# Kernel tuning notes

Hardware: AMD Instinct MI355X
Metric: run time of the kernel (lower is better)

## Reference

```python
import jax, jax.numpy as jnp
import numpy as np

B, C_IN, C_OUT, H, W = 32, 256, 256, 32, 32


def setup_inputs() -> dict:
    key = jax.random.key(0)
    kx, kw, kb = jax.random.split(key, 3)
    x = jax.random.normal(kx, (B, C_IN, H, W), dtype=jnp.float32)
    # 1x1 conv == pointwise linear over channels: weight [out_c, in_c], bias [out_c]
    conv_w = jax.random.normal(kw, (C_OUT, C_IN), dtype=jnp.float32) * (1.0 / np.sqrt(C_IN))
    conv_b = jax.random.normal(kb, (C_OUT,), dtype=jnp.float32) * 0.01
    return {"x": x, "conv_w": conv_w, "conv_b": conv_b}


def reference(x, conv_w, conv_b):
    b, c, h, w = x.shape
    hw = h * w
    q = x.reshape(b, c, hw)  # q == k == flattened x
    # score[b,i,j] = sum_c q[b,c,i] * q[b,c,j]  -> (b, hw, hw)
    score = jnp.einsum('bci,bcj->bij', q, q)
    attn = jax.nn.softmax(score, axis=-1)
    # 1x1 conv V projection: (b, out_c, h, w)
    v = jnp.einsum('oc,bchw->bohw', conv_w, x) + conv_b[None, :, None, None]
    v = v.reshape(b, -1, hw).transpose(0, 2, 1)  # (b, hw, out_c)
    out = jnp.einsum('bij,bjo->bio', attn, v)  # (b, hw, out_c)
    # torch does .transpose(-1,-1) (a no-op) then reshape(b,-1,h,w) in row-major
    out = out.reshape(b, -1, h, w)  # (b, out_c, h, w), position-major flatten as in torch
    # MaxPool2d(2): 2x2 windows, stride 2
    oc = out.shape[1]
    out = out.reshape(b, oc, h // 2, 2, w // 2, 2).max(axis=(3, 5))
    return out
```

## Files before the change

kernel.cpp:

```cpp
#include <hip/hip_runtime.h>
#include <math.h>

#define BB 32
#define CC 256
#define NN 1024
#define KSTR 264
#define PSTR 40
#define THR 8.0f

typedef unsigned short u16;
typedef u16 u16x8 __attribute__((ext_vector_type(8)));
typedef _Float16 h16;
typedef h16 h16x8 __attribute__((ext_vector_type(8)));
typedef h16 h16x4 __attribute__((ext_vector_type(4)));
typedef float f32x4 __attribute__((ext_vector_type(4)));

__device__ __forceinline__ h16x8 ldh8(const u16* p) {
    return __builtin_bit_cast(h16x8, *(const u16x8*)p);
}
__device__ __forceinline__ f32x4 mfma16(h16x8 a, h16x8 b, f32x4 c) {
    return __builtin_amdgcn_mfma_f32_16x16x32_f16(a, b, c, 0, 0, 0);
}

__global__ __launch_bounds__(256) void k_wprep(const float* __restrict__ w,
                                               u16* __restrict__ whf) {
    int s = blockIdx.x * 256 + threadIdx.x;
    int ot = s >> 9, ks = (s >> 6) & 7, l = s & 63;
    const float* src = w + (size_t)(ot * 16 + (l & 15)) * CC + ks * 32 + 8 * (l >> 4);
    float4 a = *(const float4*)src;
    float4 c = *(const float4*)(src + 4);
    u16x8 o;
    o[0] = __builtin_bit_cast(u16, (h16)a.x); o[1] = __builtin_bit_cast(u16, (h16)a.y);
    o[2] = __builtin_bit_cast(u16, (h16)a.z); o[3] = __builtin_bit_cast(u16, (h16)a.w);
    o[4] = __builtin_bit_cast(u16, (h16)c.x); o[5] = __builtin_bit_cast(u16, (h16)c.y);
    o[6] = __builtin_bit_cast(u16, (h16)c.z); o[7] = __builtin_bit_cast(u16, (h16)c.w);
    *(u16x8*)(whf + (size_t)s * 8) = o;
}

__global__ __launch_bounds__(256) void k_split(const float* __restrict__ x,
                                               u16* __restrict__ qf) {
    __shared__ float lds[64][65];
    int bid = blockIdx.x;
    int b = bid >> 6, ct = (bid >> 4) & 3, pt = bid & 15;
    int t = threadIdx.x;
    int c0 = ct * 64, p0 = pt * 64;
    const float* xb = x + ((size_t)b * CC + c0) * NN + p0;
#pragma unroll
    for (int it = 0; it < 4; ++it) {
        int cl = (t >> 4) + it * 16;
        int pl = (t & 15) * 4;
        float4 v = *(const float4*)(xb + (size_t)cl * NN + pl);
        lds[pl + 0][cl] = v.x;
        lds[pl + 1][cl] = v.y;
        lds[pl + 2][cl] = v.z;
        lds[pl + 3][cl] = v.w;
    }
    __syncthreads();
    u16* qb = qf + ((size_t)b * NN + p0) * CC + c0;
#pragma unroll
    for (int it = 0; it < 2; ++it) {
        int pl = (t >> 3) + it * 32;
        int cl = (t & 7) * 8;
        u16x8 hv;
#pragma unroll
        for (int e = 0; e < 8; ++e) hv[e] = __builtin_bit_cast(u16, (h16)lds[pl][cl + e]);
        *(u16x8*)(qb + (size_t)pl * CC + cl) = hv;
    }
}

__global__ __launch_bounds__(256, 2) void k_vgemm(const u16* __restrict__ qf,
                                                  const u16* __restrict__ whf,
                                                  const float* __restrict__ bias,
                                                  u16* __restrict__ vf) {
    __shared__ __align__(16) u16 smem[18432];
    int bid = blockIdx.x;
    int b = bid >> 4, pt = bid & 15;
    int t = threadIdx.x;
    int wave = t >> 6, lane = t & 63;
    int l15 = lane & 15, l4 = lane >> 4;
    int p0 = pt * 64, o0 = wave * 64;

#pragma unroll
    for (int it = 0; it < 8; ++it) {
        int sidx = t + it * 256;
        int row = sidx >> 5, ch = (sidx & 31) * 8;
        *(u16x8*)&smem[row * KSTR + ch] =
            *(const u16x8*)(qf + ((size_t)b * NN + p0 + row) * CC + ch);
    }
    __syncthreads();

    f32x4 acc[4][4];
#pragma unroll
    for (int m = 0; m < 4; ++m)
#pragma unroll
        for (int n = 0; n < 4; ++n) acc[m][n] = (f32x4){0.f, 0.f, 0.f, 0.f};
#pragma unroll
    for (int ks = 0; ks < 8; ++ks) {
        h16x8 afr[4], bfr[4];
#pragma unroll
        for (int m = 0; m < 4; ++m)
            afr[m] = ldh8(whf + (size_t)(((wave * 4 + m) * 8 + ks) * 64 + lane) * 8);
#pragma unroll
        for (int n = 0; n < 4; ++n)
            bfr[n] = ldh8(&smem[(n * 16 + l15) * KSTR + ks * 32 + 8 * l4]);
#pragma unroll
        for (int m = 0; m < 4; ++m)
#pragma unroll
            for (int n = 0; n < 4; ++n) acc[m][n] = mfma16(afr[m], bfr[n], acc[m][n]);
    }
    __syncthreads();

    u16* Vs = smem + wave * 4608;
#pragma unroll
    for (int m = 0; m < 4; ++m) {
#pragma unroll
        for (int r = 0; r < 4; ++r) {
            int ol = m * 16 + 4 * l4 + r;
            float bv = bias[o0 + ol];
#pragma unroll
            for (int n = 0; n < 4; ++n)
                Vs[ol * 72 + n * 16 + l15] =
                    __builtin_bit_cast(u16, (h16)(acc[m][n][r] + bv));
        }
    }
#pragma unroll
    for (int m = 0; m < 4; ++m) {
#pragma unroll
        for (int jtl = 0; jtl < 2; ++jtl) {
            u16x8 v = *(u16x8*)&Vs[(m * 16 + l15) * 72 + jtl * 32 + 8 * l4];
            size_t idx = (((size_t)b * 32 + pt * 2 + jtl) * 16 + wave * 4 + m) * 512 +
                         lane * 8;
            *(u16x8*)(vf + idx) = v;
        }
    }
}

#define SMEM_BYTES 39424
__global__ __launch_bounds__(256, 2) void k_attn(const u16* __restrict__ qf,
                                                 const u16* __restrict__ vf,
                                                 float* __restrict__ out) {
    __shared__ __align__(16) char smem[SMEM_BYTES];
    u16* Kt = (u16*)smem;
    u16* Pt = (u16*)(smem + 33792);
    float* Sc = (float*)(smem + 38912);

    int bid = blockIdx.x;
    int xcd = bid & 7, s0 = bid >> 3;
    int b = xcd * 4 + (s0 >> 4);
    int iblk = s0 & 15;
    int i0 = iblk * 64;
    int t = threadIdx.x;
    int wave = t >> 6, lane = t & 63;
    int l15 = lane & 15, l4 = lane >> 4;
    int iw = i0 + wave * 16;

    const u16* qb = qf + (size_t)b * NN * CC;
    const u16* vfb = vf + (size_t)b * (32 * 16 * 512);

    h16x8 qfr[8];
#pragma unroll
    for (int ks = 0; ks < 8; ++ks)
        qfr[ks] = ldh8(qb + (size_t)(iw + l15) * CC + ks * 32 + 8 * l4);

    f32x4 oacc[16];
#pragma unroll
    for (int i = 0; i < 16; ++i) oacc[i] = (f32x4){0.f, 0.f, 0.f, 0.f};
    float m = -INFINITY, l = 0.f;

    {
        u16x8 kp[4];
#pragma unroll
        for (int p = 0; p < 4; ++p) {
            int sidx = t + p * 256;
            kp[p] = *(const u16x8*)(qb + (size_t)(sidx >> 5) * CC + (sidx & 31) * 8);
        }
#pragma unroll
        for (int p = 0; p < 4; ++p) {
            int sidx = t + p * 256;
            *(u16x8*)&Kt[(sidx >> 5) * KSTR + (sidx & 31) * 8] = kp[p];
        }
    }
    __syncthreads();

    u16* Pw = Pt + wave * 16 * PSTR;
    float* Scw = Sc + wave * 16;

    for (int jt = 0; jt < 32; ++jt) {
        int cur = jt & 1;
        int j0 = jt * 32;
        const u16* Kc = Kt + cur * (32 * KSTR) + l15 * KSTR + 8 * l4;

        u16x8 vfr[16];
#pragma unroll
        for (int of = 0; of < 16; ++of)
            vfr[of] = *(const u16x8*)(vfb + ((size_t)(jt * 16 + of) * 512 + lane * 8));

        u16x8 kp[4];
        if (jt < 31) {
#pragma unroll
            for (int p = 0; p < 4; ++p) {
                int sidx = t + p * 256;
                kp[p] = *(const u16x8*)(qb + (size_t)(j0 + 32 + (sidx >> 5)) * CC +
                                        (sidx & 31) * 8);
            }
        }

        f32x4 s0v = (f32x4){0.f, 0.f, 0.f, 0.f};
        f32x4 s1v = (f32x4){0.f, 0.f, 0.f, 0.f};
#pragma unroll
        for (int ks = 0; ks < 8; ++ks) {
            h16x8 a0 = ldh8(Kc + ks * 32);
            h16x8 a1 = ldh8(Kc + 16 * KSTR + ks * 32);
            s0v = mfma16(a0, qfr[ks], s0v);
            s1v = mfma16(a1, qfr[ks], s1v);
        }

        float mx = fmaxf(fmaxf(fmaxf(s0v[0], s0v[1]), fmaxf(s0v[2], s0v[3])),
                         fmaxf(fmaxf(s1v[0], s1v[1]), fmaxf(s1v[2], s1v[3])));
        mx = fmaxf(mx, __shfl_xor(mx, 16));
        mx = fmaxf(mx, __shfl_xor(mx, 32));
        if (__any(mx > m + THR)) {
            float mnew = fmaxf(m, mx);
            float sc = __expf(m - mnew);
            m = mnew;
            l *= sc;
            Scw[l15] = sc;
            f32x4 s4 = *(f32x4*)&Scw[4 * l4];
#pragma unroll
            for (int of = 0; of < 16; ++of)
#pragma unroll
                for (int r = 0; r < 4; ++r) oacc[of][r] *= s4[r];
        }
        float p0 = __expf(s0v[0] - m), p1 = __expf(s0v[1] - m);
        float p2 = __expf(s0v[2] - m), p3 = __expf(s0v[3] - m);
        float p4 = __expf(s1v[0] - m), p5 = __expf(s1v[1] - m);
        float p6 = __expf(s1v[2] - m), p7 = __expf(s1v[3] - m);
        float rs = ((p0 + p1) + (p2 + p3)) + ((p4 + p5) + (p6 + p7));
        rs += __shfl_xor(rs, 16);
        rs += __shfl_xor(rs, 32);
        l += rs;

        h16x4 pk0 = {(h16)p0, (h16)p1, (h16)p2, (h16)p3};
        h16x4 pk1 = {(h16)p4, (h16)p5, (h16)p6, (h16)p7};
        *(h16x4*)(Pw + l15 * PSTR + 4 * l4) = pk0;
        *(h16x4*)(Pw + l15 * PSTR + 16 + 4 * l4) = pk1;
        h16x8 pa = ldh8(Pw + l15 * PSTR + 8 * l4);

#pragma unroll
        for (int of = 0; of < 16; ++of)
            oacc[of] = mfma16(pa, __builtin_bit_cast(h16x8, vfr[of]), oacc[of]);

        if (jt < 31) {
#pragma unroll
            for (int p = 0; p < 4; ++p) {
                int sidx = t + p * 256;
                *(u16x8*)&Kt[(cur ^ 1) * (32 * KSTR) + (sidx >> 5) * KSTR +
                             (sidx & 31) * 8] = kp[p];
            }
            __syncthreads();
        }
    }

    {
        float inv = 1.0f / l;
        Scw[l15] = inv;
        f32x4 inv4 = *(f32x4*)&Scw[4 * l4];
#pragma unroll
        for (int of = 0; of < 16; ++of)
#pragma unroll
            for (int r = 0; r < 4; ++r) oacc[of][r] *= inv4[r];
    }

    float* Old = (float*)smem;
#pragma unroll
    for (int half = 0; half < 2; ++half) {
        __syncthreads();
        if ((wave >> 1) == half) {
            int wrow = (wave & 1) * 16;
#pragma unroll
            for (int of = 0; of < 16; ++of)
#pragma unroll
                for (int r = 0; r < 4; ++r)
                    Old[(wrow + 4 * l4 + r) * 260 + of * 16 + l15] = oacc[of][r];
        }
        __syncthreads();
#pragma unroll
        for (int it = 0; it < 8; ++it) {
            int q = it * 16 + (t >> 4);
            int ill = q >> 2, pl = q & 3, pw = t & 15;
            const float* row = &Old[ill * 260];
            int ob = pl * 64 + pw * 2;
            float mx = fmaxf(fmaxf(row[ob], row[ob + 1]),
                             fmaxf(row[ob + 32], row[ob + 33]));
            int i = i0 + half * 32 + ill;
            out[(((size_t)b * CC + (i >> 2)) * 16 + (i & 3) * 4 + pl) * 16 + pw] = mx;
        }
    }
}

extern "C" void kernel_launch(void* const* d_in, const int* in_sizes, int n_in,
                              void* d_out, int out_size, void* d_ws, size_t ws_size,
                              hipStream_t stream) {
    const float* x = (const float*)d_in[0];
    const float* w = (const float*)d_in[1];
    const float* bias = (const float*)d_in[2];
    float* out = (float*)d_out;
    u16* qf = (u16*)d_ws;
    u16* vf = qf + (size_t)BB * NN * CC;
    u16* whf = vf + (size_t)BB * NN * CC;
    k_wprep<<<32, 256, 0, stream>>>(w, whf);
    k_split<<<2048, 256, 0, stream>>>(x, qf);
    k_vgemm<<<512, 256, 0, stream>>>(qf, whf, bias, vf);
    k_attn<<<512, 256, 0, stream>>>(qf, vf, out);
}
```

Baseline: 147.6 us.

## Fuse transpose/convert with V projection and stage K via direct global-to-LDS loads

Merges the x transpose/fp16 conversion kernel and the V-projection GEMM into a single kernel. It computes V directly from fp32 x tiles held in LDS, which removes one launch and the round trip through qf for the GEMM. In the attention kernel, K tiles are now staged with global_load_lds into an unpadded, XOR-swizzled layout instead of going through registers, which frees VGPRs and drops the explicit LDS stores. The risks are the swizzle's bank-conflict behaviour and the vmcnt/barrier ordering needed before the async LDS writes become visible.

```diff
diff --git a/kernel.cpp b/kernel.cpp
--- a/kernel.cpp
+++ b/kernel.cpp
@@ -4,11 +4,12 @@
 #define BB 32
 #define CC 256
 #define NN 1024
-#define KSTR 264
+#define KSTR 256
 #define PSTR 40
 #define THR 8.0f
 
 typedef unsigned short u16;
+typedef unsigned int u32;
 typedef u16 u16x8 __attribute__((ext_vector_type(8)));
 typedef _Float16 h16;
 typedef h16 h16x8 __attribute__((ext_vector_type(8)));
@@ -20,6 +21,10 @@
 }
 __device__ __forceinline__ f32x4 mfma16(h16x8 a, h16x8 b, f32x4 c) {
     return __builtin_amdgcn_mfma_f32_16x16x32_f16(a, b, c, 0, 0, 0);
+}
+__device__ __forceinline__ void gll16(const void* g, void* l) {
+    __builtin_amdgcn_global_load_lds((const __attribute__((address_space(1))) u32*)g,
+                                     (__attribute__((address_space(3))) u32*)l, 16, 0, 0);
 }
 
 __global__ __launch_bounds__(256) void k_wprep(const float* __restrict__ w,
@@ -37,126 +42,121 @@
     *(u16x8*)(whf + (size_t)s * 8) = o;
 }
 
-__global__ __launch_bounds__(256) void k_split(const float* __restrict__ x,
-                                               u16* __restrict__ qf) {
-    __shared__ float lds[64][65];
-    int bid = blockIdx.x;
-    int b = bid >> 6, ct = (bid >> 4) & 3, pt = bid & 15;
-    int t = threadIdx.x;
-    int c0 = ct * 64, p0 = pt * 64;
-    const float* xb = x + ((size_t)b * CC + c0) * NN + p0;
-#pragma unroll
-    for (int it = 0; it < 4; ++it) {
-        int cl = (t >> 4) + it * 16;
-        int pl = (t & 15) * 4;
-        float4 v = *(const float4*)(xb + (size_t)cl * NN + pl);
-        lds[pl + 0][cl] = v.x;
-        lds[pl + 1][cl] = v.y;
-        lds[pl + 2][cl] = v.z;
-        lds[pl + 3][cl] = v.w;
-    }
-    __syncthreads();
-    u16* qb = qf + ((size_t)b * NN + p0) * CC + c0;
-#pragma unroll
-    for (int it = 0; it < 2; ++it) {
-        int pl = (t >> 3) + it * 32;
-        int cl = (t & 7) * 8;
-        u16x8 hv;
-#pragma unroll
-        for (int e = 0; e < 8; ++e) hv[e] = __builtin_bit_cast(u16, (h16)lds[pl][cl + e]);
-        *(u16x8*)(qb + (size_t)pl * CC + cl) = hv;
-    }
-}
-
-__global__ __launch_bounds__(256, 2) void k_vgemm(const u16* __restrict__ qf,
+__global__ __launch_bounds__(256, 4) void k_xform(const float* __restrict__ x,
                                                   const u16* __restrict__ whf,
                                                   const float* __restrict__ bias,
+                                                  u16* __restrict__ qf,
                                                   u16* __restrict__ vf) {
-    __shared__ __align__(16) u16 smem[18432];
+    __shared__ __align__(16) float xs[32][68];
+    __shared__ __align__(16) u16 Vs[4][64 * 40];
     int bid = blockIdx.x;
-    int b = bid >> 4, pt = bid & 15;
-    int t = threadIdx.x;
-    int wave = t >> 6, lane = t & 63;
+    int b = bid >> 5, pt = bid & 31;
+    int t = threadIdx.x, wave = t >> 6, lane = t & 63;
     int l15 = lane & 15, l4 = lane >> 4;
-    int p0 = pt * 64, o0 = wave * 64;
-
-#pragma unroll
-    for (int it = 0; it < 8; ++it) {
-        int sidx = t + it * 256;
-        int row = sidx >> 5, ch = (sidx & 31) * 8;
-        *(u16x8*)&smem[row * KSTR + ch] =
-            *(const u16x8*)(qf + ((size_t)b * NN + p0 + row) * CC + ch);
-    }
-    __syncthreads();
-
-    f32x4 acc[4][4];
+    int p0 = pt * 32;
+
+    f32x4 acc[4][2];
 #pragma unroll
     for (int m = 0; m < 4; ++m)
 #pragma unroll
-        for (int n = 0; n < 4; ++n) acc[m][n] = (f32x4){0.f, 0.f, 0.f, 0.f};
-#pragma unroll
-    for (int ks = 0; ks < 8; ++ks) {
-        h16x8 afr[4], bfr[4];
-#pragma unroll
-        for (int m = 0; m < 4; ++m)
-            afr[m] = ldh8(whf + (size_t)(((wave * 4 + m) * 8 + ks) * 64 + lane) * 8);
-#pragma unroll
-        for (int n = 0; n < 4; ++n)
-            bfr[n] = ldh8(&smem[(n * 16 + l15) * KSTR + ks * 32 + 8 * l4]);
-#pragma unroll
-        for (int m = 0; m < 4; ++m)
-#pragma unroll
-            for (int n = 0; n < 4; ++n) acc[m][n] = mfma16(afr[m], bfr[n], acc[m][n]);
-    }
-    __syncthreads();
-
-    u16* Vs = smem + wave * 4608;
+        for (int n = 0; n < 2; ++n) acc[m][n] = (f32x4){0.f, 0.f, 0.f, 0.f};
+
+    for (int cc = 0; cc < 4; ++cc) {
+#pragma unroll
+        for (int it = 0; it < 2; ++it) {
+            int r = (t >> 3) + it * 32;
+            int pq = (t & 7) * 4;
+            float4 v = *(const float4*)(x + (size_t)(b * CC + cc * 64 + r) * NN + p0 + pq);
+            xs[pq + 0][r] = v.x;
+            xs[pq + 1][r] = v.y;
+            xs[pq + 2][r] = v.z;
+            xs[pq + 3][r] = v.w;
+        }
+        __syncthreads();
+        {
+            int p = t >> 3, cl = (t & 7) * 8;
+            u16x8 hv;
+#pragma unroll
+            for (int e = 0; e < 8; ++e)
+                hv[e] = __builtin_bit_cast(u16, (h16)xs[p][cl + e]);
+            *(u16x8*)(qf + (size_t)(b * NN + p0 + p) * CC + cc * 64 + cl) = hv;
+        }
+#pragma unroll
+        for (int ksl = 0; ksl < 2; ++ksl) {
+            int ks = cc * 2 + ksl;
+            h16x8 afr[4], bfr[2];
+#pragma unroll
+            for (int m = 0; m < 4; ++m)
+                afr[m] = ldh8(whf + (size_t)(((wave * 4 + m) * 8 + ks) * 64 + lane) * 8);
+#pragma unroll
+            for (int n = 0; n < 2; ++n) {
+                const float* sp = &xs[n * 16 + l15][ksl * 32 + 8 * l4];
+                f32x4 w0 = *(const f32x4*)sp;
+                f32x4 w1 = *(const f32x4*)(sp + 4);
+                h16x8 tv;
+                tv[0] = (h16)w0[0]; tv[1] = (h16)w0[1]; tv[2] = (h16)w0[2]; tv[3] = (h16)w0[3];
+                tv[4] = (h16)w1[0]; tv[5] = (h16)w1[1]; tv[6] = (h16)w1[2]; tv[7] = (h16)w1[3];
+                bfr[n] = tv;
+            }
+#pragma unroll
+            for (int m = 0; m < 4; ++m)
+#pragma unroll
+                for (int n = 0; n < 2; ++n) acc[m][n] = mfma16(afr[m], bfr[n], acc[m][n]);
+        }
+        __syncthreads();
+    }
+
+    u16* Vsw = &Vs[wave][0];
 #pragma unroll
     for (int m = 0; m < 4; ++m) {
 #pragma unroll
         for (int r = 0; r < 4; ++r) {
             int ol = m * 16 + 4 * l4 + r;
-            float bv = bias[o0 + ol];
-#pragma unroll
-            for (int n = 0; n < 4; ++n)
-                Vs[ol * 72 + n * 16 + l15] =
+            float bv = bias[wave * 64 + ol];
+#pragma unroll
+            for (int n = 0; n < 2; ++n)
+                Vsw[ol * 40 + n * 16 + l15] =
                     __builtin_bit_cast(u16, (h16)(acc[m][n][r] + bv));
         }
     }
 #pragma unroll
     for (int m = 0; m < 4; ++m) {
-#pragma unroll
-        for (int jtl = 0; jtl < 2; ++jtl) {
-            u16x8 v = *(u16x8*)&Vs[(m * 16 + l15) * 72 + jtl * 32 + 8 * l4];
-            size_t idx = (((size_t)b * 32 + pt * 2 + jtl) * 16 + wave * 4 + m) * 512 +
-                         lane * 8;
-            *(u16x8*)(vf + idx) = v;
-        }
-    }
-}
-
-#define SMEM_BYTES 39424
+        u16x8 v = *(u16x8*)&Vsw[(m * 16 + l15) * 40 + 8 * l4];
+        *(u16x8*)(vf + (((size_t)(b * 32 + pt) * 16) + wave * 4 + m) * 512 + lane * 8) = v;
+    }
+}
+
+#define SMEM_BYTES 38400
 __global__ __launch_bounds__(256, 2) void k_attn(const u16* __restrict__ qf,
                                                  const u16* __restrict__ vf,
                                                  float* __restrict__ out) {
     __shared__ __align__(16) char smem[SMEM_BYTES];
     u16* Kt = (u16*)smem;
-    u16* Pt = (u16*)(smem + 33792);
-    float* Sc = (float*)(smem + 38912);
+    u16* Pt = (u16*)(smem + 32768);
+    float* Sc = (float*)(smem + 37888);
 
     int bid = blockIdx.x;
     int xcd = bid & 7, s0 = bid >> 3;
     int b = xcd * 4 + (s0 >> 4);
-    int iblk = s0 & 15;
-    int i0 = iblk * 64;
-    int t = threadIdx.x;
-    int wave = t >> 6, lane = t & 63;
-    int l15 = lane & 15, l4 = lane >> 4;
+    int i0 = (s0 & 15) * 64;
+    int t = threadIdx.x, wave = t >> 6, lane = t & 63;
+    int l15 = lane & 15, l4 = lane >> 4, l7 = lane & 7;
     int iw = i0 + wave * 16;
 
     const u16* qb = qf + (size_t)b * NN * CC;
     const u16* vfb = vf + (size_t)b * (32 * 16 * 512);
 
+#define STAGE_K(J0, BUF)                                                        \
+    {                                                                           \
+        int Gb = wave * 4;                                                      \
+        _Pragma("unroll") for (int inst = 0; inst < 4; ++inst) {                \
+            int G = (Gb + inst) * 64 + lane;                                    \
+            int row = G >> 5, g = G & 31;                                       \
+            gll16(qb + (size_t)((J0) + row) * CC + ((g ^ (row & 7)) << 3),      \
+                  Kt + (BUF) * 8192 + (size_t)(Gb + inst) * 512);               \
+        }                                                                       \
+    }
+
     h16x8 qfr[8];
 #pragma unroll
     for (int ks = 0; ks < 8; ++ks)
@@ -167,19 +167,7 @@
     for (int i = 0; i < 16; ++i) oacc[i] = (f32x4){0.f, 0.f, 0.f, 0.f};
     float m = -INFINITY, l = 0.f;
 
-    {
-        u16x8 kp[4];
-#pragma unroll
-        for (int p = 0; p < 4; ++p) {
-            int sidx = t + p * 256;
-            kp[p] = *(const u16x8*)(qb + (size_t)(sidx >> 5) * CC + (sidx & 31) * 8);
-        }
-#pragma unroll
-        for (int p = 0; p < 4; ++p) {
-            int sidx = t + p * 256;
-            *(u16x8*)&Kt[(sidx >> 5) * KSTR + (sidx & 31) * 8] = kp[p];
-        }
-    }
+    STAGE_K(0, 0);
     __syncthreads();
 
     u16* Pw = Pt + wave * 16 * PSTR;
@@ -188,29 +176,22 @@
     for (int jt = 0; jt < 32; ++jt) {
         int cur = jt & 1;
         int j0 = jt * 32;
-        const u16* Kc = Kt + cur * (32 * KSTR) + l15 * KSTR + 8 * l4;
 
         u16x8 vfr[16];
 #pragma unroll
         for (int of = 0; of < 16; ++of)
             vfr[of] = *(const u16x8*)(vfb + ((size_t)(jt * 16 + of) * 512 + lane * 8));
 
-        u16x8 kp[4];
-        if (jt < 31) {
-#pragma unroll
-            for (int p = 0; p < 4; ++p) {
-                int sidx = t + p * 256;
-                kp[p] = *(const u16x8*)(qb + (size_t)(j0 + 32 + (sidx >> 5)) * CC +
-                                        (sidx & 31) * 8);
-            }
-        }
-
+        if (jt < 31) STAGE_K(j0 + 32, cur ^ 1);
+
+        const u16* KtC = Kt + cur * 8192 + l15 * KSTR;
         f32x4 s0v = (f32x4){0.f, 0.f, 0.f, 0.f};
         f32x4 s1v = (f32x4){0.f, 0.f, 0.f, 0.f};
 #pragma unroll
         for (int ks = 0; ks < 8; ++ks) {
-            h16x8 a0 = ldh8(Kc + ks * 32);
-            h16x8 a1 = ldh8(Kc + 16 * KSTR + ks * 32);
+            int g0 = ((4 * ks + l4) ^ l7) << 3;
+            h16x8 a0 = ldh8(KtC + g0);
+            h16x8 a1 = ldh8(KtC + 16 * KSTR + g0);
             s0v = mfma16(a0, qfr[ks], s0v);
             s1v = mfma16(a1, qfr[ks], s1v);
         }
@@ -250,15 +231,7 @@
         for (int of = 0; of < 16; ++of)
             oacc[of] = mfma16(pa, __builtin_bit_cast(h16x8, vfr[of]), oacc[of]);
 
-        if (jt < 31) {
-#pragma unroll
-            for (int p = 0; p < 4; ++p) {
-                int sidx = t + p * 256;
-                *(u16x8*)&Kt[(cur ^ 1) * (32 * KSTR) + (sidx >> 5) * KSTR +
-                             (sidx & 31) * 8] = kp[p];
-            }
-            __syncthreads();
-        }
+        if (jt < 31) __syncthreads();
     }
 
     {
@@ -290,10 +263,10 @@
             int ill = q >> 2, pl = q & 3, pw = t & 15;
             const float* row = &Old[ill * 260];
             int ob = pl * 64 + pw * 2;
-            float mx = fmaxf(fmaxf(row[ob], row[ob + 1]),
-                             fmaxf(row[ob + 32], row[ob + 33]));
+            float mx2 = fmaxf(fmaxf(row[ob], row[ob + 1]),
+                              fmaxf(row[ob + 32], row[ob + 33]));
             int i = i0 + half * 32 + ill;
-            out[(((size_t)b * CC + (i >> 2)) * 16 + (i & 3) * 4 + pl) * 16 + pw] = mx;
+            out[(((size_t)b * CC + (i >> 2)) * 16 + (i & 3) * 4 + pl) * 16 + pw] = mx2;
         }
     }
 }
@@ -309,7 +282,6 @@
     u16* vf = qf + (size_t)BB * NN * CC;
     u16* whf = vf + (size_t)BB * NN * CC;
     k_wprep<<<32, 256, 0, stream>>>(w, whf);
-    k_split<<<2048, 256, 0, stream>>>(x, qf);
-    k_vgemm<<<512, 256, 0, stream>>>(qf, whf, bias, vf);
+    k_xform<<<1024, 256, 0, stream>>>(x, whf, bias, qf, vf);
     k_attn<<<512, 256, 0, stream>>>(qf, vf, out);
 }
```

Result: faster. 144.0 us (-2.4%).
